# Optimization experiments

Measured on AMD Instinct MI355X. Metric: run time of the kernel, lower is better.

Reference implementation:

```python
import jax, jax.numpy as jnp
import numpy as np
from itertools import combinations

SEQ_LEN = 10; WAY = 5; SHOT = 5; TSS = 2
IN_DIM = 2048; OUT_DIM = 2048
PAIRS = np.array(list(combinations(range(SEQ_LEN), TSS)))  # [T, 2] frame-pair indices
T = PAIRS.shape[0]  # 45 tuples


def _cdist(a, b):
    # Euclidean distance matrix, stable form: sqrt(|a|^2 + |b|^2 - 2 a.b)
    a2 = jnp.sum(a * a, axis=-1)[:, None]
    b2 = jnp.sum(b * b, axis=-1)[None, :]
    sq = a2 + b2 - 2.0 * (a @ b.T)
    return jnp.sqrt(jnp.maximum(sq, 0.0))


def setup_inputs() -> dict:
    key = jax.random.key(0)
    k1, k2, k3, k4 = jax.random.split(key, 4)
    n_s = WAY * SHOT            # 25
    n_q = WAY * 15              # 75
    support_set = jax.random.normal(k1, (n_s, SEQ_LEN, IN_DIM), jnp.float32)
    queries = jax.random.normal(k2, (n_q, SEQ_LEN, IN_DIM), jnp.float32)
    # class-sorted labels: class c occupies rows [c*SHOT, (c+1)*SHOT)
    support_labels = jnp.arange(n_s, dtype=jnp.int32) // SHOT
    lim = 1.0 / np.sqrt(IN_DIM * TSS)
    clsW_w = jax.random.uniform(k3, (OUT_DIM, IN_DIM * TSS), jnp.float32, -lim, lim)
    clsW_b = jax.random.uniform(k4, (OUT_DIM,), jnp.float32, -lim, lim)
    return {"support_set": support_set, "support_labels": support_labels,
            "queries": queries, "clsW_w": clsW_w, "clsW_b": clsW_b}


def _forward(support_set, queries, clsW_w, clsW_b):
    n_s, n_q = support_set.shape[0], queries.shape[0]
    D2 = TSS * IN_DIM
    # tuple gather: [n, T, 2*in_dim] (dropout is eval-mode identity)
    sup = support_set[:, PAIRS, :].reshape(n_s, T, D2)
    qry = queries[:, PAIRS, :].reshape(n_q, T, D2)
    q_embed = jax.nn.relu(qry.reshape(n_q * T, D2) @ clsW_w.T + clsW_b)      # [nqT, D]
    sup_c = sup.reshape(WAY, SHOT * T, D2)                                    # labels sorted by class
    support_all = jax.nn.relu(jnp.einsum('csd,od->cso', sup_c, clsW_w) + clsW_b)  # [way, sT, D]

    distmat = jax.vmap(lambda s: _cdist(q_embed, s))(support_all)             # [way, nqT, sT]
    # torch: view(-1, T, shot).topk(k=1, dim=1).mean -> max over reshaped axis
    dist_class = distmat.reshape(WAY, n_q * T, T, SHOT).max(axis=2)           # [way, nqT, shot]
    ave_dist_all = dist_class.mean(axis=2)                                    # [way, nqT]
    dist_min = distmat.min(axis=2).reshape(WAY, n_q, T).mean(axis=2).T        # [n_q, way] (computed, unused downstream)
    dist_max = distmat.max(axis=2).reshape(WAY, n_q, T).mean(axis=2).T        # [n_q, way]
    pos_all = jnp.argmax(distmat, axis=2)                                     # [way, nqT]

    cols = []
    for c in range(WAY):
        mse = support_all[c][pos_all[c]]                                      # [nqT, D]
        other = support_all[np.array([m for m in range(WAY) if m != c])]      # [way-1, sT, D]
        other_flat = other.reshape((WAY - 1) * SHOT * T, OUT_DIM)
        cosd = _cdist(mse, other_flat).reshape(n_q * T, WAY - 1, SHOT * T)
        cosd = cosd.transpose(1, 0, 2)                                        # [way-1, nqT, sT]
        # record_pos[idx, s2] = #{s1 : cosd[idx,s1,s2] > ave_dist_all[c, s1]}
        record = jnp.sum(cosd > ave_dist_all[c][None, :, None], axis=1).astype(jnp.float32)  # [way-1, sT]
        nz = jnp.maximum(jnp.sum(record != 0, axis=1), 1).astype(jnp.float32)
        thr = record.sum(axis=1) / nz                                         # mean over nonzero entries
        mask = (record < thr[:, None]).astype(jnp.float32)                    # selected columns per other-class
        # diff_embed = concat of selected rows; mean of cdist over them == masked mean
        d_full = _cdist(q_embed, other_flat)                                  # [nqT, (way-1)*sT]
        msum = jnp.maximum(mask.sum(), 1.0)
        mean_d = (d_full * mask.reshape(-1)[None, :]).sum(axis=1) / msum      # [nqT]
        cols.append(mean_d.reshape(n_q, T).mean(axis=1) / (WAY - 1))
    dist_contrast = jnp.stack(cols, axis=1)                                   # [n_q, way]

    logits_contrast = dist_max / (dist_contrast + dist_max)
    return dist_max, logits_contrast


def reference(support_set, support_labels, queries, clsW_w, clsW_b):
    # support_labels are sorted class blocks (arange // shot); class gather is a reshape
    return _forward(support_set, queries, clsW_w, clsW_b)
```

## Files before the change

### kernel.cpp

```cpp
#include <hip/hip_runtime.h>


typedef __bf16 bf16x8 __attribute__((ext_vector_type(8)));
typedef float f32x4 __attribute__((ext_vector_type(4)));

#define NQT   3375
#define MROWS 4500
#define MPAD  4608
#define LDD   1152
#define BK    32

__constant__ int P0[45] = {0,0,0,0,0,0,0,0,0,
                           1,1,1,1,1,1,1,1,
                           2,2,2,2,2,2,2,
                           3,3,3,3,3,3,
                           4,4,4,4,4,
                           5,5,5,5,
                           6,6,6,
                           7,7,
                           8};
__constant__ int P1[45] = {1,2,3,4,5,6,7,8,9,
                           2,3,4,5,6,7,8,9,
                           3,4,5,6,7,8,9,
                           4,5,6,7,8,9,
                           5,6,7,8,9,
                           6,7,8,9,
                           7,8,9,
                           8,9,
                           9};

__device__ inline unsigned short f2b(float x) {
  __bf16 b = (__bf16)x;
  return __builtin_bit_cast(unsigned short, b);
}
__device__ inline float b2f(unsigned int u16) {
  return __uint_as_float(u16 << 16);
}

__device__ __forceinline__ void gl_lds16(const unsigned short* g, unsigned short* l) {
  __builtin_amdgcn_global_load_lds(
      (__attribute__((address_space(1))) void*)(g),
      (__attribute__((address_space(3))) void*)(l),
      16, 0, 0);
}

__global__ void prep(const float* __restrict__ W, const float* __restrict__ Q,
                     const float* __restrict__ Sp,
                     unsigned short* __restrict__ Ws, unsigned short* __restrict__ X,
                     float* __restrict__ record, float* __restrict__ sq) {
  int b = blockIdx.x, tid = threadIdx.x;
  if (b < 8192) {
    int i = b * 256 + tid;
    int i4 = i << 2;
    int o  = i4 >> 12;
    int k  = i4 & 4095;
    int hf = k >> 11;
    int kk = k & 2047;
    float4 v = reinterpret_cast<const float4*>(W)[i];
    ushort4 u;
    u.x = f2b(v.x); u.y = f2b(v.y); u.z = f2b(v.z); u.w = f2b(v.w);
    *reinterpret_cast<ushort4*>(Ws + (size_t)(o + hf * 2048) * 2048 + kk) = u;
  } else if (b < 10240) {
    int i = (b - 8192) * 256 + tid;
    ushort4 u = {0, 0, 0, 0};
    if (i < 384000) {
      float4 v = reinterpret_cast<const float4*>(Q)[i];
      u.x = f2b(v.x); u.y = f2b(v.y); u.z = f2b(v.z); u.w = f2b(v.w);
    } else if (i < 512000) {
      float4 v = reinterpret_cast<const float4*>(Sp)[i - 384000];
      u.x = f2b(v.x); u.y = f2b(v.y); u.z = f2b(v.z); u.w = f2b(v.w);
    }
    reinterpret_cast<ushort4*>(X)[i] = u;
  } else {
    int i = (b - 10240) * 256 + tid;
    if (i < 4500) record[i] = 0.f;
    else if (i < 4500 + 4608) sq[i - 4500] = 0.f;
  }
}

__global__ __launch_bounds__(512)
void gemm_ring(const unsigned short* __restrict__ A, const unsigned short* __restrict__ B,
               int lda, int ldb, int Ksplit,
               float* __restrict__ Pout0, float* __restrict__ Pout1, int ldd) {
  __shared__ unsigned short As[4][128 * BK];
  __shared__ unsigned short Bs[4][128 * BK];
  const int tid  = threadIdx.x;
  const int wave = tid >> 6, lane = tid & 63;
  const int quad = lane >> 4, l16 = lane & 15;
  const int wm = (wave >> 2) * 64, wn = (wave & 3) * 32;
  const int m0 = blockIdx.x * 128, n0 = blockIdx.y * 128;
  const int kbase = blockIdx.z * Ksplit;

  f32x4 acc[4][2];
#pragma unroll
  for (int i = 0; i < 4; ++i)
#pragma unroll
    for (int j = 0; j < 2; ++j) {
      f32x4 z = {0.f, 0.f, 0.f, 0.f};
      acc[i][j] = z;
    }

  const int r0  = tid >> 2;
  const int qsw = (tid & 3) ^ ((tid >> 3) & 3);
  const int kp0 = qsw * 8;
  const int rsw = (quad ^ ((l16 >> 1) & 3)) * 8;
  const unsigned short* pa = A + (size_t)(m0 + r0) * lda + kbase + kp0;
  const unsigned short* pb = B + (size_t)(n0 + r0) * ldb + kbase + kp0;
  const int NKi = Ksplit / BK;

#define ISSUE(kk, st) do {                                 \
    gl_lds16(pa + (size_t)(kk) * BK, &As[st][wave * 512]); \
    gl_lds16(pb + (size_t)(kk) * BK, &Bs[st][wave * 512]); \
  } while (0)

  ISSUE(0, 0);
  ISSUE(1, 1);
  ISSUE(2, 2);
  asm volatile("s_waitcnt vmcnt(4)" ::: "memory");
  __builtin_amdgcn_s_barrier();

  for (int k = 0; k < NKi; ++k) {
    if (k + 3 < NKi) ISSUE(k + 3, (k + 3) & 3);
    const int sc = k & 3;
    bf16x8 af[4], bfr[2];
#pragma unroll
    for (int t = 0; t < 4; ++t)
      af[t] = *reinterpret_cast<const bf16x8*>(&As[sc][(wm + t * 16 + l16) * BK + rsw]);
#pragma unroll
    for (int t = 0; t < 2; ++t)
      bfr[t] = *reinterpret_cast<const bf16x8*>(&Bs[sc][(wn + t * 16 + l16) * BK + rsw]);
#pragma unroll
    for (int i = 0; i < 4; ++i)
#pragma unroll
      for (int j = 0; j < 2; ++j)
        acc[i][j] = __builtin_amdgcn_mfma_f32_16x16x32_bf16(af[i], bfr[j], acc[i][j], 0, 0, 0);
    if (k + 1 < NKi) {
      if (k + 3 < NKi)      asm volatile("s_waitcnt vmcnt(4)" ::: "memory");
      else if (k + 2 < NKi) asm volatile("s_waitcnt vmcnt(2)" ::: "memory");
      else                  asm volatile("s_waitcnt vmcnt(0)" ::: "memory");
      __builtin_amdgcn_s_barrier();
    }
  }
#undef ISSUE
  asm volatile("s_waitcnt vmcnt(0)" ::: "memory");

  float* Pout = blockIdx.z ? Pout1 : Pout0;
#pragma unroll
  for (int i = 0; i < 4; ++i)
#pragma unroll
    for (int j = 0; j < 2; ++j) {
      int col = n0 + wn + j * 16 + l16;
      int rbase = m0 + wm + i * 16 + quad * 4;
      f32x4 v = acc[i][j];
#pragma unroll
      for (int r = 0; r < 4; ++r)
        Pout[(size_t)(rbase + r) * ldd + col] = v[r];
    }
}

__global__ __launch_bounds__(256)
void build_e2(const float* __restrict__ Y0, const float* __restrict__ Y1,
              const float* __restrict__ bias,
              unsigned short* __restrict__ E, float* __restrict__ sq) {
  int b = blockIdx.x, tid = threadIdx.x;
  if (b >= 400) {
    const size_t base = (size_t)4500 * 2048 / 8;
    const int total = 108 * 2048 / 8;
    uint4 z = {0, 0, 0, 0};
    for (int i = (b - 400) * 256 + tid; i < total; i += 512)
      reinterpret_cast<uint4*>(E)[base + i] = z;
    return;
  }
  int n = b >> 2, q = b & 3;
  int c0 = q * 512;
  __shared__ float Lf[10][512];
  __shared__ float Rf[10][512];
  for (int e = tid; e < 1280; e += 256) {
    int f  = e >> 7;
    int cc = (e & 127) << 2;
    const float* ya = Y0 + (size_t)(n * 10 + f) * 4096;
    const float* yb = Y1 + (size_t)(n * 10 + f) * 4096;
    float4 l0 = *reinterpret_cast<const float4*>(ya + c0 + cc);
    float4 l1 = *reinterpret_cast<const float4*>(yb + c0 + cc);
    float4 r0 = *reinterpret_cast<const float4*>(ya + 2048 + c0 + cc);
    float4 r1 = *reinterpret_cast<const float4*>(yb + 2048 + c0 + cc);
    float4 L = {l0.x + l1.x, l0.y + l1.y, l0.z + l1.z, l0.w + l1.w};
    float4 R = {r0.x + r1.x, r0.y + r1.y, r0.z + r1.z, r0.w + r1.w};
    *reinterpret_cast<float4*>(&Lf[f][cc]) = L;
    *reinterpret_cast<float4*>(&Rf[f][cc]) = R;
  }
  __syncthreads();
  int wv = tid >> 6, lane = tid & 63;
  int erow0 = (n < 75) ? n * 45 : NQT + (n - 75) * 45;
  for (int t = wv; t < 45; t += 4) {
    int f0 = P0[t], f1 = P1[t];
    int row = erow0 + t;
    float s = 0.f;
#pragma unroll
    for (int k = 0; k < 8; ++k) {
      int c = lane + 64 * k;
      float x = Lf[f0][c] + Rf[f1][c] + bias[c0 + c];
      x = fmaxf(x, 0.f);
      unsigned short ob = f2b(x);
      E[(size_t)row * 2048 + c0 + c] = ob;
      float xr = b2f(ob);
      s += xr * xr;
    }
#pragma unroll
    for (int sh = 32; sh > 0; sh >>= 1) s += __shfl_down(s, sh, 64);
    if (lane == 0) atomicAdd(&sq[row], s);
  }
}

__global__ __launch_bounds__(320)
void dist_stats(const float* __restrict__ Pa, const float* __restrict__ Pb,
                const float* __restrict__ sq, float* __restrict__ D,
                float* __restrict__ ave, int* __restrict__ pos,
                float* __restrict__ rmax) {
  __shared__ float drow[LDD];
  __shared__ float sm[5][64];
  int row = blockIdx.x, tid = threadIdx.x;
  float sr = sq[row];
  if (tid < 288) {
    int c = tid * 4;
    size_t ix = (size_t)row * LDD / 4 + tid;
    float4 a = reinterpret_cast<const float4*>(Pa)[ix];
    float4 bb = reinterpret_cast<const float4*>(Pb)[ix];
    float4 o;
    o.x = sqrtf(fmaxf(sr + sq[NQT + c + 0] - 2.f * (a.x + bb.x), 0.f));
    o.y = sqrtf(fmaxf(sr + sq[NQT + c + 1] - 2.f * (a.y + bb.y), 0.f));
    o.z = sqrtf(fmaxf(sr + sq[NQT + c + 2] - 2.f * (a.z + bb.z), 0.f));
    o.w = sqrtf(fmaxf(sr + sq[NQT + c + 3] - 2.f * (a.w + bb.w), 0.f));
    reinterpret_cast<float4*>(D)[ix] = o;
    *reinterpret_cast<float4*>(&drow[c]) = o;
  }
  __syncthreads();
  if (row >= NQT) return;
  int wv = tid >> 6, lane = tid & 63;
  const float* p = &drow[wv * 225];
  float best = -1e30f; int bi = 225;
  float gm = -1e30f;
  if (lane < 60) {
#pragma unroll
    for (int r = 0; r < 4; ++r) {
      int j = lane + 60 * r;
      if (j < 225) {
        float v = p[j];
        if (v > best) { best = v; bi = j; }
        gm = fmaxf(gm, v);
      }
    }
  }
#pragma unroll
  for (int s = 32; s > 0; s >>= 1) {
    float vv = __shfl_down(best, s, 64);
    int   ii = __shfl_down(bi,   s, 64);
    if (vv > best || (vv == best && ii < bi)) { best = vv; bi = ii; }
  }
  sm[wv][lane] = gm;
  __builtin_amdgcn_wave_barrier();
  if (lane < 5) {
    float m = -1e30f;
#pragma unroll
    for (int a = 0; a < 12; ++a) m = fmaxf(m, sm[wv][lane + 5 * a]);
    sm[wv][lane] = m;
  }
  __builtin_amdgcn_wave_barrier();
  if (lane == 0) {
    float s5 = sm[wv][0] + sm[wv][1] + sm[wv][2] + sm[wv][3] + sm[wv][4];
    ave[wv * NQT + row]  = s5 * 0.2f;
    pos[wv * NQT + row]  = bi;
    rmax[wv * NQT + row] = best;
  }
}

__global__ void record_part(const float* __restrict__ D, const float* __restrict__ ave,
                            const int* __restrict__ pos, float* __restrict__ record) {
  int b = blockIdx.x;
  int c = b / 135, chunk = b - c * 135;
  int i0 = chunk * 25;
  int tid = threadIdx.x;
  __shared__ int   sp[25];
  __shared__ float sa[25];
  if (tid < 25) {
    sp[tid] = pos[c * NQT + i0 + tid];
    sa[tid] = ave[c * NQT + i0 + tid];
  }
  __syncthreads();
  float cnt[4] = {0.f, 0.f, 0.f, 0.f};
  int gcol[4];
#pragma unroll
  for (int j = 0; j < 4; ++j) {
    int col = tid + j * 256;
    gcol[j] = (col < 900) ? (col < c * 225 ? col : col + 225) : 0;
  }
  const bool act3 = (tid + 768) < 900;
  const float* Dsup = D + (size_t)(NQT + c * 225) * LDD;
  for (int ii = 0; ii < 25; ++ii) {
    const float* row = Dsup + (size_t)sp[ii] * LDD;
    float a = sa[ii];
    cnt[0] += (row[gcol[0]] > a) ? 1.f : 0.f;
    cnt[1] += (row[gcol[1]] > a) ? 1.f : 0.f;
    cnt[2] += (row[gcol[2]] > a) ? 1.f : 0.f;
    if (act3) cnt[3] += (row[gcol[3]] > a) ? 1.f : 0.f;
  }
#pragma unroll
  for (int j = 0; j < 4; ++j) {
    int col = tid + j * 256;
    if (col < 900) atomicAdd(&record[c * 900 + col], cnt[j]);
  }
}

__global__ __launch_bounds__(256)
void tail_fused(const float* __restrict__ D, const float* __restrict__ record,
                const float* __restrict__ rmax, float* __restrict__ out) {
  int q = blockIdx.x;
  int tid = threadIdx.x;
  int wv = tid >> 6, lane = tid & 63;
  __shared__ float maskT[5 * LDD];
  __shared__ float msum_s[5];
  __shared__ float St[5][45];
  for (int i = tid; i < 5 * LDD; i += 256) maskT[i] = 0.f;
  if (tid < 5) msum_s[tid] = 0.f;
  __syncthreads();

  for (int seg = wv; seg < 20; seg += 4) {
    int c = seg >> 2, mi = seg & 3;
    const float* rec = record + c * 900 + mi * 225;
    float r0 = (lane < 225) ? rec[lane] : 0.f;
    float r1 = rec[lane + 64];
    float r2 = rec[lane + 128];
    float r3 = (lane + 192 < 225) ? rec[lane + 192] : 0.f;
    float s  = r0 + r1 + r2 + r3;
    float nz = (r0 != 0.f ? 1.f : 0.f) + (r1 != 0.f ? 1.f : 0.f) +
               (r2 != 0.f ? 1.f : 0.f) + (r3 != 0.f ? 1.f : 0.f);
#pragma unroll
    for (int sh = 32; sh > 0; sh >>= 1) {
      s  += __shfl_down(s,  sh, 64);
      nz += __shfl_down(nz, sh, 64);
    }
    s  = __shfl(s,  0, 64);
    nz = __shfl(nz, 0, 64);
    float nzc = nz < 1.f ? 1.f : nz;
    float thr = s / nzc;
    float mcount = 0.f;
    float rv[4] = {r0, r1, r2, r3};
#pragma unroll
    for (int j = 0; j < 4; ++j) {
      int idx = lane + j * 64;
      if (idx < 225) {
        float m = (rv[j] < thr) ? 1.f : 0.f;
        int L = mi * 225 + idx;
        int g = L + (L >= c * 225 ? 225 : 0);
        maskT[c * LDD + g] = m;
        mcount += m;
      }
    }
#pragma unroll
    for (int sh = 32; sh > 0; sh >>= 1) mcount += __shfl_down(mcount, sh, 64);
    if (lane == 0) atomicAdd(&msum_s[c], mcount);
  }
  __syncthreads();

  for (int t = wv; t < 45; t += 4) {
    const float* row = D + (size_t)(q * 45 + t) * LDD;
    float a0 = 0.f, a1 = 0.f, a2 = 0.f, a3 = 0.f, a4 = 0.f;
#pragma unroll
    for (int k = 0; k < 18; ++k) {
      int col = k * 64 + lane;
      float d = row[col];
      a0 += d * maskT[0 * LDD + col];
      a1 += d * maskT[1 * LDD + col];
      a2 += d * maskT[2 * LDD + col];
      a3 += d * maskT[3 * LDD + col];
      a4 += d * maskT[4 * LDD + col];
    }
#pragma unroll
    for (int sh = 32; sh > 0; sh >>= 1) {
      a0 += __shfl_down(a0, sh, 64);
      a1 += __shfl_down(a1, sh, 64);
      a2 += __shfl_down(a2, sh, 64);
      a3 += __shfl_down(a3, sh, 64);
      a4 += __shfl_down(a4, sh, 64);
    }
    if (lane == 0) {
      St[0][t] = a0; St[1][t] = a1; St[2][t] = a2; St[3][t] = a3; St[4][t] = a4;
    }
  }
  __syncthreads();

  if (tid < 5) {
    int c = tid;
    float dsum = 0.f, ssum = 0.f;
    for (int t = 0; t < 45; ++t) {
      dsum += rmax[c * NQT + q * 45 + t];
      ssum += St[c][t];
    }
    float dm = dsum / 45.f;
    float ms = msum_s[c]; if (ms < 1.f) ms = 1.f;
    float contrast = ssum / (ms * 180.f);
    out[q * 5 + c] = dm;
    out[375 + q * 5 + c] = dm / (contrast + dm);
  }
}

extern "C" void kernel_launch(void* const* d_in, const int* in_sizes, int n_in,
                              void* d_out, int out_size, void* d_ws, size_t ws_size,
                              hipStream_t stream) {
  const float* support = (const float*)d_in[0];
  const float* queries = (const float*)d_in[2];
  const float* W       = (const float*)d_in[3];
  const float* bias    = (const float*)d_in[4];
  float* out = (float*)d_out;

  char* ws = (char*)d_ws;
  size_t off = 0;
  unsigned short* Xb  = (unsigned short*)(ws + off);
  unsigned short* Wsp = (unsigned short*)(ws + off + 4194304);
  float*          Pd1 = (float*)(ws + off);          off += 21233664;
  float*          Y0  = (float*)(ws + off);          off += (size_t)1024 * 4096 * 4;
  float*          Dm  = (float*)(ws + off);
  float*          Y1  = (float*)(ws + off);          off += (size_t)MPAD * LDD * 4;
  unsigned short* Eb  = (unsigned short*)(ws + off); off += (size_t)MPAD * 2048 * 2;
  float* sq      = (float*)(ws + off); off += 4608 * 4 + 256;
  float* ave     = (float*)(ws + off); off += 5 * NQT * 4 + 256;
  int*   pos     = (int*)(ws + off);   off += 5 * NQT * 4 + 256;
  float* rmax    = (float*)(ws + off); off += 5 * NQT * 4 + 256;
  float* record  = (float*)(ws + off); off += 5 * 900 * 4 + 256;

  prep<<<10276, 256, 0, stream>>>(W, queries, support, Wsp, Xb, record, sq);

  dim3 g1(1024 / 128, 4096 / 128, 2);
  gemm_ring<<<g1, 512, 0, stream>>>(Xb, Wsp, 2048, 2048, 1024, Y0, Y1, 4096);

  build_e2<<<402, 256, 0, stream>>>(Y0, Y1, bias, Eb, sq);

  dim3 g2(MPAD / 128, LDD / 128, 2);
  gemm_ring<<<g2, 512, 0, stream>>>(Eb, Eb + (size_t)NQT * 2048, 2048, 2048, 1024,
                                    Dm, Pd1, LDD);

  dist_stats<<<MROWS, 320, 0, stream>>>(Dm, Pd1, sq, Dm, ave, pos, rmax);

  record_part<<<675, 256, 0, stream>>>(Dm, ave, pos, record);
  tail_fused<<<75, 256, 0, stream>>>(Dm, record, rmax, out);
}
```

Baseline: 228.8 us.

## Swizzle GEMM workgroups across XCDs and process two K-tiles per barrier

The GEMM kernel remaps its linear workgroup index so that consecutive tiles are spread across the 8 chiplets. This aims to improve L2 locality of shared A/B panels. The K loop now handles two BK tiles per iteration, issuing the next two tile loads up front and using a single full vmcnt wait plus one barrier per pair. That halves the barrier count but drops the finer-grained three-deep prefetch, so less memory latency may be hidden. The mapping is only a bijection when the total block count is divisible by 8. A redundant bounds check in the tail kernel is also removed.

```diff
diff --git a/kernel.cpp b/kernel.cpp
--- a/kernel.cpp
+++ b/kernel.cpp
@@ -88,8 +88,19 @@
   const int wave = tid >> 6, lane = tid & 63;
   const int quad = lane >> 4, l16 = lane & 15;
   const int wm = (wave >> 2) * 64, wn = (wave & 3) * 32;
-  const int m0 = blockIdx.x * 128, n0 = blockIdx.y * 128;
-  const int kbase = blockIdx.z * Ksplit;
+
+  const int gx = gridDim.x, gy = gridDim.y;
+  const int nwg = gx * gy * gridDim.z;
+  const int lin = blockIdx.x + gx * (blockIdx.y + gy * blockIdx.z);
+  const int cpx = nwg >> 3;
+  const int swz = (lin & 7) * cpx + (lin >> 3);
+  const int bz  = swz / (gx * gy);
+  const int rem = swz - bz * gx * gy;
+  const int by  = rem / gx;
+  const int bx  = rem - by * gx;
+
+  const int m0 = bx * 128, n0 = by * 128;
+  const int kbase = bz * Ksplit;
 
   f32x4 acc[4][2];
 #pragma unroll
@@ -115,36 +126,45 @@
 
   ISSUE(0, 0);
   ISSUE(1, 1);
-  ISSUE(2, 2);
-  asm volatile("s_waitcnt vmcnt(4)" ::: "memory");
+  asm volatile("s_waitcnt vmcnt(0)" ::: "memory");
   __builtin_amdgcn_s_barrier();
 
-  for (int k = 0; k < NKi; ++k) {
-    if (k + 3 < NKi) ISSUE(k + 3, (k + 3) & 3);
-    const int sc = k & 3;
-    bf16x8 af[4], bfr[2];
-#pragma unroll
-    for (int t = 0; t < 4; ++t)
-      af[t] = *reinterpret_cast<const bf16x8*>(&As[sc][(wm + t * 16 + l16) * BK + rsw]);
-#pragma unroll
-    for (int t = 0; t < 2; ++t)
-      bfr[t] = *reinterpret_cast<const bf16x8*>(&Bs[sc][(wn + t * 16 + l16) * BK + rsw]);
+  for (int kp = 0; kp < NKi; kp += 2) {
+    if (kp + 2 < NKi) {
+      ISSUE(kp + 2, (kp + 2) & 3);
+      ISSUE(kp + 3, (kp + 3) & 3);
+    }
+    const int s0 = kp & 3, s1 = s0 | 1;
+    bf16x8 a0[4], a1[4], b0[2], b1[2];
+#pragma unroll
+    for (int t = 0; t < 4; ++t) {
+      a0[t] = *reinterpret_cast<const bf16x8*>(&As[s0][(wm + t * 16 + l16) * BK + rsw]);
+      a1[t] = *reinterpret_cast<const bf16x8*>(&As[s1][(wm + t * 16 + l16) * BK + rsw]);
+    }
+#pragma unroll
+    for (int t = 0; t < 2; ++t) {
+      b0[t] = *reinterpret_cast<const bf16x8*>(&Bs[s0][(wn + t * 16 + l16) * BK + rsw]);
+      b1[t] = *reinterpret_cast<const bf16x8*>(&Bs[s1][(wn + t * 16 + l16) * BK + rsw]);
+    }
 #pragma unroll
     for (int i = 0; i < 4; ++i)
 #pragma unroll
       for (int j = 0; j < 2; ++j)
-        acc[i][j] = __builtin_amdgcn_mfma_f32_16x16x32_bf16(af[i], bfr[j], acc[i][j], 0, 0, 0);
-    if (k + 1 < NKi) {
-      if (k + 3 < NKi)      asm volatile("s_waitcnt vmcnt(4)" ::: "memory");
-      else if (k + 2 < NKi) asm volatile("s_waitcnt vmcnt(2)" ::: "memory");
-      else                  asm volatile("s_waitcnt vmcnt(0)" ::: "memory");
+        acc[i][j] = __builtin_amdgcn_mfma_f32_16x16x32_bf16(a0[i], b0[j], acc[i][j], 0, 0, 0);
+#pragma unroll
+    for (int i = 0; i < 4; ++i)
+#pragma unroll
+      for (int j = 0; j < 2; ++j)
+        acc[i][j] = __builtin_amdgcn_mfma_f32_16x16x32_bf16(a1[i], b1[j], acc[i][j], 0, 0, 0);
+    if (kp + 2 < NKi) {
+      asm volatile("s_waitcnt vmcnt(0)" ::: "memory");
       __builtin_amdgcn_s_barrier();
     }
   }
 #undef ISSUE
   asm volatile("s_waitcnt vmcnt(0)" ::: "memory");
 
-  float* Pout = blockIdx.z ? Pout1 : Pout0;
+  float* Pout = bz ? Pout1 : Pout0;
 #pragma unroll
   for (int i = 0; i < 4; ++i)
 #pragma unroll
@@ -327,7 +347,7 @@
   for (int seg = wv; seg < 20; seg += 4) {
     int c = seg >> 2, mi = seg & 3;
     const float* rec = record + c * 900 + mi * 225;
-    float r0 = (lane < 225) ? rec[lane] : 0.f;
+    float r0 = rec[lane];
     float r1 = rec[lane + 64];
     float r2 = rec[lane + 128];
     float r3 = (lane + 192 < 225) ? rec[lane + 192] : 0.f;
```

Measured after the change: 215.3 us. 1.06x faster.
